# Kernel tuning notes

Hardware: AMD Instinct MI355X
Metric: run time of the kernel (lower is better)

Reference implementation:

```python
import jax, jax.numpy as jnp
import numpy as np


def _l2norm(v, eps=1e-12):
    # torch F.normalize(dim=-1): v / clamp(||v||_2, min=eps)
    n = jnp.linalg.norm(v, axis=-1, keepdims=True)
    return v / jnp.maximum(n, eps)


def setup_inputs() -> dict:
    key = jax.random.key(0)
    ks = jax.random.split(key, 10)
    B, T, N, Ci, E, K, H = 64, 12, 1024, 64, 16, 3, 192
    O = H // 3  # subhidden size
    return {
        "x": jax.random.normal(ks[0], (B, N, Ci), jnp.float32),
        "x_window": jax.random.normal(ks[1], (B, T, N, 1), jnp.float32),
        "node_embeddings": jax.random.normal(ks[2], (N, E), jnp.float32) * 0.1,
        "ZPI": jax.random.normal(ks[3], (B, 3), jnp.float32),
        "supports_adj": jax.random.uniform(ks[4], (K, N, N), jnp.float32),
        "weights_pool": jax.random.normal(ks[5], (E, K, Ci, O), jnp.float32) * 0.1,
        "weights_pool_adj": jax.random.normal(ks[6], (E, K, Ci, O), jnp.float32) * 0.1,
        "weights_window": jax.random.normal(ks[7], (E, 1, O), jnp.float32) * 0.1,
        "bias_pool": jax.random.normal(ks[8], (E, H), jnp.float32) * 0.1,
        "T_param": jax.random.normal(ks[9], (T,), jnp.float32) * 0.1,
    }


def reference(x, x_window, node_embeddings, ZPI, supports_adj,
              weights_pool, weights_pool_adj, weights_window, bias_pool, T_param):
    N = node_embeddings.shape[0]
    K = weights_pool.shape[1]  # link_len

    # adaptive supports: softmax(relu(E E^T)) and its power series
    supports = jax.nn.softmax(jax.nn.relu(node_embeddings @ node_embeddings.T), axis=1)
    support_set = [jnp.eye(N, dtype=x.dtype), supports]
    for k in range(2, K):
        support_set.append(supports @ support_set[k - 1])
    S = jnp.stack(support_set, axis=0)  # (K, N, N)

    # per-node dynamic weights / bias
    weights = jnp.einsum('nd,dkio->nkio', node_embeddings, weights_pool)
    bias = node_embeddings @ bias_pool  # (N, H)

    # adaptive graph conv branch
    x_g = jnp.einsum('knm,bmc->bnkc', S, x)
    x_gconv = _l2norm(jnp.einsum('bnki,nkio->bno', x_g, weights))

    # static adjacency branch ('knn' repeated index = diagonal; sum over m --
    # faithful to the original torch einsum)
    weights_adj = jnp.einsum('nd,dkio->nkio', node_embeddings, weights_pool_adj)
    x_a = jnp.einsum('knn,bmc->bnkc', supports_adj, x)
    x_aconv = _l2norm(jnp.einsum('bnki,nkio->bno', x_a, weights_adj))

    # temporal window branch
    ww = jnp.einsum('nd,dio->nio', node_embeddings, weights_window)  # (N, 1, O)
    x_w = jnp.einsum('btni,nio->btno', x_window, ww)
    x_wconv = _l2norm(jnp.einsum('btno,t->bno', x_w, T_param))

    return jnp.concatenate([x_gconv, x_aconv, x_wconv], axis=-1) + bias
```

## Files before the change

### kernel.cpp

```cpp
#include <hip/hip_runtime.h>


typedef __attribute__((ext_vector_type(4))) float f32x4;
typedef __attribute__((ext_vector_type(8))) short short8;

#define DEVI static __device__ __forceinline__

DEVI float bf2f(short u) {
    unsigned int x = ((unsigned int)(unsigned short)u) << 16;
    return __builtin_bit_cast(float, x);
}
DEVI short f2bf(float f) {
    unsigned int x = __builtin_bit_cast(unsigned int, f);
    x = (x + 0x7FFFu + ((x >> 16) & 1u)) >> 16;
    return (short)(unsigned short)x;
}
DEVI int swz(int row) { return ((row ^ (row >> 3)) & 7) << 3; }

DEVI f32x4 mfma16(short8 a, short8 b, f32x4 c) {
    return __builtin_amdgcn_mfma_f32_16x16x32_bf16(a, b, c, 0, 0, 0);
}

__global__ __launch_bounds__(256) void k_supports(const float* __restrict__ NE,
                                                  short* __restrict__ A_bf) {
    int n = blockIdx.x, t = threadIdx.x;
    __shared__ float En[16];
    __shared__ float wsum[4];
    if (t < 16) En[t] = NE[n * 16 + t];
    __syncthreads();
    float e[4];
    float loc = 0.f;
#pragma unroll
    for (int i = 0; i < 4; ++i) {
        int m = t + 256 * i;
        const float* rp = NE + m * 16;
        float v = 0.f;
#pragma unroll
        for (int d = 0; d < 16; ++d) v += En[d] * rp[d];
        v = fmaxf(v, 0.f);
        e[i] = __expf(v);
        loc += e[i];
    }
#pragma unroll
    for (int off = 32; off; off >>= 1) loc += __shfl_xor(loc, off);
    if ((t & 63) == 0) wsum[t >> 6] = loc;
    __syncthreads();
    float inv = 1.f / (wsum[0] + wsum[1] + wsum[2] + wsum[3]);
#pragma unroll
    for (int i = 0; i < 4; ++i) A_bf[n * 1024 + t + 256 * i] = f2bf(e[i] * inv);
}

__global__ __launch_bounds__(256) void k_small(
        const float* __restrict__ x, const float* __restrict__ xw,
        const float* __restrict__ NE, const float* __restrict__ adj,
        const float* __restrict__ wp, const float* __restrict__ wpa,
        const float* __restrict__ Tp,
        short* __restrict__ B2, short* __restrict__ A2,
        float* __restrict__ xsp, float* __restrict__ s_bn) {
    __shared__ float red[4][64];
    int bid = blockIdx.x, t = threadIdx.x;
    if (bid < 64) {
        int o = bid, j = t;
        short row[64];
        if (j < 192) {
            int kk = j >> 6, i = j & 63;
#pragma unroll
            for (int d = 0; d < 16; ++d)
                row[d] = f2bf(wp[((d * 3 + kk) * 64 + i) * 64 + o]);
#pragma unroll
            for (int k = 16; k < 64; ++k) row[k] = 0;
        } else {
            int i2 = j - 192;
#pragma unroll
            for (int k = 0; k < 16; ++k) row[k] = 0;
#pragma unroll
            for (int d = 0; d < 16; ++d)
#pragma unroll
                for (int kk = 0; kk < 3; ++kk)
                    row[16 + d * 3 + kk] = f2bf(wpa[((d * 3 + kk) * 64 + i2) * 64 + o]);
        }
        short* dst = B2 + (o * 256 + j) * 64;
#pragma unroll
        for (int q = 0; q < 8; ++q) {
            short8 v;
#pragma unroll
            for (int e2 = 0; e2 < 8; ++e2) v[e2] = row[q * 8 + e2];
            *reinterpret_cast<short8*>(dst + q * 8) = v;
        }
    } else if (bid < 320) {
        int idx = bid - 64, b = idx >> 2, mq = idx & 3;
        int c = t & 63, q2 = t >> 6;
        int m0 = mq * 256 + q2 * 64;
        float s = 0.f;
        for (int mm = 0; mm < 64; ++mm) s += x[(b * 1024 + m0 + mm) * 64 + c];
        red[q2][c] = s;
        __syncthreads();
        if (t < 64) xsp[(b * 4 + mq) * 64 + t] = red[0][t] + red[1][t] + red[2][t] + red[3][t];
    } else if (bid < 336) {
        int idx = bid - 320;
        float tp[12];
#pragma unroll
        for (int i = 0; i < 12; ++i) tp[i] = Tp[i];
        for (int bb = 0; bb < 4; ++bb) {
            int b = idx * 4 + bb;
#pragma unroll
            for (int j2 = 0; j2 < 4; ++j2) {
                int nn = t + 256 * j2;
                float s = 0.f;
#pragma unroll
                for (int tt = 0; tt < 12; ++tt) s += xw[(b * 12 + tt) * 1024 + nn] * tp[tt];
                s_bn[b * 1024 + nn] = s;
            }
        }
    } else {
        int n = (bid - 336) * 256 + t;
        float En[16];
#pragma unroll
        for (int d = 0; d < 16; ++d) En[d] = NE[n * 16 + d];
        float dg[3];
#pragma unroll
        for (int k = 0; k < 3; ++k) dg[k] = adj[k * 1024 * 1024 + n * 1024 + n];
        short row[64];
#pragma unroll
        for (int d = 0; d < 16; ++d) row[d] = f2bf(En[d]);
#pragma unroll
        for (int d = 0; d < 16; ++d)
#pragma unroll
            for (int k = 0; k < 3; ++k) row[16 + d * 3 + k] = f2bf(En[d] * dg[k]);
        short* dst = A2 + n * 64;
#pragma unroll
        for (int q = 0; q < 8; ++q) {
            short8 v;
#pragma unroll
            for (int e2 = 0; e2 < 8; ++e2) v[e2] = row[q * 8 + e2];
            *reinterpret_cast<short8*>(dst + q * 8) = v;
        }
    }
}

__global__ __launch_bounds__(256) void k_gemm_w(const short* __restrict__ A2,
                                                const short* __restrict__ B2,
                                                short* __restrict__ Wall) {
    int bx = blockIdx.x, by = blockIdx.y;
    __shared__ __align__(16) short As[128 * 64];
    __shared__ __align__(16) short Bs[128 * 64];
    int t = threadIdx.x;
#pragma unroll
    for (int i = 0; i < 4; ++i) {
        int slot = t + 256 * i;
        int row = slot >> 3, k8 = slot & 7;
        int sw = swz(row);
        short8 va = *reinterpret_cast<const short8*>(A2 + (by * 128 + row) * 64 + k8 * 8);
        *reinterpret_cast<short8*>(&As[row * 64 + ((k8 * 8) ^ sw)]) = va;
        short8 vb = *reinterpret_cast<const short8*>(B2 + (bx * 128 + row) * 64 + k8 * 8);
        *reinterpret_cast<short8*>(&Bs[row * 64 + ((k8 * 8) ^ sw)]) = vb;
    }
    __syncthreads();
    int w = t >> 6, l = t & 63;
    int wm = w & 1, wn = w >> 1;
    int lr = l & 15, lg = l >> 4;
    f32x4 acc[4][4] = {};
#pragma unroll
    for (int ks = 0; ks < 2; ++ks) {
        int kk = ks * 32 + lg * 8;
        short8 af[4], bfr[4];
#pragma unroll
        for (int mf = 0; mf < 4; ++mf) {
            int row = wm * 64 + mf * 16 + lr;
            af[mf] = *reinterpret_cast<const short8*>(&As[row * 64 + (kk ^ swz(row))]);
        }
#pragma unroll
        for (int nf = 0; nf < 4; ++nf) {
            int row = wn * 64 + nf * 16 + lr;
            bfr[nf] = *reinterpret_cast<const short8*>(&Bs[row * 64 + (kk ^ swz(row))]);
        }
#pragma unroll
        for (int mf = 0; mf < 4; ++mf)
#pragma unroll
            for (int nf = 0; nf < 4; ++nf)
                acc[mf][nf] = mfma16(af[mf], bfr[nf], acc[mf][nf]);
    }
#pragma unroll
    for (int mf = 0; mf < 4; ++mf)
#pragma unroll
        for (int nf = 0; nf < 4; ++nf)
#pragma unroll
            for (int r = 0; r < 4; ++r) {
                int row = by * 128 + wm * 64 + mf * 16 + lg * 4 + r;
                int col = bx * 128 + wn * 64 + nf * 16 + lr;
                Wall[row * 16384 + col] = f2bf(acc[mf][nf][r]);
            }
}

template <int BF32>
__global__ __launch_bounds__(256) void k_gemm(const short* __restrict__ A_bf,
                                              const void* __restrict__ Bsrc,
                                              short* __restrict__ Crm) {
    int n0 = blockIdx.x * 128, b = blockIdx.y;
    __shared__ __align__(16) short As[128 * 64];
    __shared__ __align__(16) short Bs[64 * 64];
    int t = threadIdx.x;
    int w = t >> 6, l = t & 63;
    int wm = w & 1, wn = w >> 1;
    int lr = l & 15, lg = l >> 4;
    f32x4 acc[4][2] = {};
    const float* Bf = reinterpret_cast<const float*>(Bsrc) + b * 65536;
    const short* Bh = reinterpret_cast<const short*>(Bsrc) + b * 65536;
    int arow = t >> 3, ak8 = t & 7;
    int bc0 = (t & 7) * 8, bm = t >> 3;
    for (int kt = 0; kt < 16; ++kt) {
#pragma unroll
        for (int i = 0; i < 4; ++i) {
            int row = arow + 32 * i;
            short8 v = *reinterpret_cast<const short8*>(
                A_bf + (n0 + row) * 1024 + kt * 64 + ak8 * 8);
            *reinterpret_cast<short8*>(&As[row * 64 + ((ak8 * 8) ^ swz(row))]) = v;
        }
#pragma unroll
        for (int it = 0; it < 2; ++it) {
            int m = bm + 32 * it;
            if (BF32) {
                const float4* p = reinterpret_cast<const float4*>(Bf + (kt * 64 + m) * 64 + bc0);
                float4 p0 = p[0], p1 = p[1];
                float vv[8] = {p0.x, p0.y, p0.z, p0.w, p1.x, p1.y, p1.z, p1.w};
#pragma unroll
                for (int j = 0; j < 8; ++j) {
                    int c = bc0 + j;
                    Bs[c * 64 + (m ^ swz(c))] = f2bf(vv[j]);
                }
            } else {
                short8 hv = *reinterpret_cast<const short8*>(Bh + (kt * 64 + m) * 64 + bc0);
#pragma unroll
                for (int j = 0; j < 8; ++j) {
                    int c = bc0 + j;
                    Bs[c * 64 + (m ^ swz(c))] = hv[j];
                }
            }
        }
        __syncthreads();
#pragma unroll
        for (int ks = 0; ks < 2; ++ks) {
            int kk = ks * 32 + lg * 8;
            short8 af[4], bfr[2];
#pragma unroll
            for (int mf = 0; mf < 4; ++mf) {
                int row = wm * 64 + mf * 16 + lr;
                af[mf] = *reinterpret_cast<const short8*>(&As[row * 64 + (kk ^ swz(row))]);
            }
#pragma unroll
            for (int nf = 0; nf < 2; ++nf) {
                int c = wn * 32 + nf * 16 + lr;
                bfr[nf] = *reinterpret_cast<const short8*>(&Bs[c * 64 + (kk ^ swz(c))]);
            }
#pragma unroll
            for (int mf = 0; mf < 4; ++mf)
#pragma unroll
                for (int nf = 0; nf < 2; ++nf)
                    acc[mf][nf] = mfma16(af[mf], bfr[nf], acc[mf][nf]);
        }
        __syncthreads();
    }
#pragma unroll
    for (int mf = 0; mf < 4; ++mf)
#pragma unroll
        for (int nf = 0; nf < 2; ++nf)
#pragma unroll
            for (int r = 0; r < 4; ++r) {
                int nrow = n0 + wm * 64 + mf * 16 + lg * 4 + r;
                int c = wn * 32 + nf * 16 + lr;
                Crm[(b * 1024 + nrow) * 64 + c] = f2bf(acc[mf][nf][r]);
            }
}

__global__ __launch_bounds__(256) void k_epi(
        const float* __restrict__ x, const short* __restrict__ y1,
        const short* __restrict__ y2, const float* __restrict__ xsp,
        const float* __restrict__ s_bn, const short* __restrict__ Wall,
        const float* __restrict__ NE, const float* __restrict__ bp,
        const float* __restrict__ wwin, float* __restrict__ out) {
    int n = blockIdx.x, t = threadIdx.x;
    __shared__ __align__(16) short Ylds[64 * 256];
    __shared__ float E_l[16];
    __shared__ float bias_l[192];
    __shared__ float ww_l[64];
    __shared__ float sq_l[2][2][64];
    __shared__ float wwn_l;
    if (t < 16) E_l[t] = NE[n * 16 + t];
    __syncthreads();
    if (t < 192) {
        float s = 0.f;
#pragma unroll
        for (int d = 0; d < 16; ++d) s += E_l[d] * bp[d * 192 + t];
        bias_l[t] = s;
    } else {
        int o = t - 192;
        float s = 0.f;
#pragma unroll
        for (int d = 0; d < 16; ++d) s += E_l[d] * wwin[d * 64 + o];
        ww_l[o] = s;
    }
    int w = t >> 6, l = t & 63;
    int wm = w & 1, wn = w >> 1;
    int lr = l & 15, lg = l >> 4;
    short8 wf[8][2];
#pragma unroll
    for (int ks = 0; ks < 8; ++ks)
#pragma unroll
        for (int nf = 0; nf < 2; ++nf) {
            int o = wn * 32 + nf * 16 + lr;
            int k = ks * 32 + lg * 8;
            wf[ks][nf] = *reinterpret_cast<const short8*>(Wall + (n * 64 + o) * 256 + k);
        }
    for (int it = 0; it < 16; ++it) {
        int b = it * 4 + (t >> 6);
        int c = t & 63;
        int sw = swz(b);
        int base = b * 256;
        float xv = x[(b * 1024 + n) * 64 + c];
        short y1v = y1[(b * 1024 + n) * 64 + c];
        short y2v = y2[(b * 1024 + n) * 64 + c];
        float xs = xsp[(b * 4 + 0) * 64 + c] + xsp[(b * 4 + 1) * 64 + c] +
                   xsp[(b * 4 + 2) * 64 + c] + xsp[(b * 4 + 3) * 64 + c];
        Ylds[base + ((0 * 64 + c) ^ sw)] = f2bf(xv);
        Ylds[base + ((1 * 64 + c) ^ sw)] = y1v;
        Ylds[base + ((2 * 64 + c) ^ sw)] = y2v;
        Ylds[base + ((3 * 64 + c) ^ sw)] = f2bf(xs);
    }
    __syncthreads();
    if (t < 64) {
        float v = ww_l[t];
        float s2 = v * v;
#pragma unroll
        for (int off = 32; off; off >>= 1) s2 += __shfl_xor(s2, off);
        if (t == 0) wwn_l = sqrtf(s2);
    }
    f32x4 accg[2][2] = {};
    f32x4 acca[2][2] = {};
#pragma unroll
    for (int ks = 0; ks < 8; ++ks) {
        short8 af[2];
#pragma unroll
        for (int mf = 0; mf < 2; ++mf) {
            int b = wm * 32 + mf * 16 + lr;
            int k = ks * 32 + lg * 8;
            af[mf] = *reinterpret_cast<const short8*>(&Ylds[b * 256 + (k ^ swz(b))]);
        }
#pragma unroll
        for (int mf = 0; mf < 2; ++mf)
#pragma unroll
            for (int nf = 0; nf < 2; ++nf) {
                if (ks < 6) accg[mf][nf] = mfma16(af[mf], wf[ks][nf], accg[mf][nf]);
                else        acca[mf][nf] = mfma16(af[mf], wf[ks][nf], acca[mf][nf]);
            }
    }
#pragma unroll
    for (int mf = 0; mf < 2; ++mf)
#pragma unroll
        for (int r = 0; r < 4; ++r) {
            float sg = accg[mf][0][r] * accg[mf][0][r] + accg[mf][1][r] * accg[mf][1][r];
            float sa = acca[mf][0][r] * acca[mf][0][r] + acca[mf][1][r] * acca[mf][1][r];
#pragma unroll
            for (int off = 1; off < 16; off <<= 1) {
                sg += __shfl_xor(sg, off);
                sa += __shfl_xor(sa, off);
            }
            if (lr == 0) {
                int b = wm * 32 + mf * 16 + lg * 4 + r;
                sq_l[0][wn][b] = sg;
                sq_l[1][wn][b] = sa;
            }
        }
    __syncthreads();
#pragma unroll
    for (int mf = 0; mf < 2; ++mf)
#pragma unroll
        for (int r = 0; r < 4; ++r) {
            int b = wm * 32 + mf * 16 + lg * 4 + r;
            float ig = 1.f / fmaxf(sqrtf(sq_l[0][0][b] + sq_l[0][1][b]), 1e-12f);
            float ia = 1.f / fmaxf(sqrtf(sq_l[1][0][b] + sq_l[1][1][b]), 1e-12f);
            float* po = out + (b * 1024 + n) * 192;
#pragma unroll
            for (int nf = 0; nf < 2; ++nf) {
                int o = wn * 32 + nf * 16 + lr;
                po[o]      = accg[mf][nf][r] * ig + bias_l[o];
                po[64 + o] = acca[mf][nf][r] * ia + bias_l[64 + o];
            }
        }
    float wwn = wwn_l;
    for (int it = 0; it < 16; ++it) {
        int b = it * 4 + (t >> 6);
        int o = t & 63;
        float s = s_bn[b * 1024 + n];
        float pre = s * ww_l[o];
        float nrm = fabsf(s) * wwn;
        out[(b * 1024 + n) * 192 + 128 + o] = pre / fmaxf(nrm, 1e-12f) + bias_l[128 + o];
    }
}

extern "C" void kernel_launch(void* const* d_in, const int* in_sizes, int n_in,
                              void* d_out, int out_size, void* d_ws, size_t ws_size,
                              hipStream_t stream) {
    const float* x    = (const float*)d_in[0];
    const float* xw   = (const float*)d_in[1];
    const float* NE   = (const float*)d_in[2];
    const float* adj  = (const float*)d_in[4];
    const float* wp   = (const float*)d_in[5];
    const float* wpa  = (const float*)d_in[6];
    const float* wwin = (const float*)d_in[7];
    const float* bp   = (const float*)d_in[8];
    const float* Tp   = (const float*)d_in[9];
    float* out = (float*)d_out;

    char* ws = (char*)d_ws;
    const size_t OFF_ABF  = 0;
    const size_t OFF_Y1   = 2097152;
    const size_t OFF_Y2   = 10485760;
    const size_t OFF_WALL = 18874368;
    const size_t OFF_A2   = 52428800;
    const size_t OFF_B2   = 52559872;
    const size_t OFF_XSP  = 54657024;
    const size_t OFF_SBN  = 54722560;
    const size_t NEED     = 54984704;
    if (ws_size < NEED) return;

    short* A_bf = (short*)(ws + OFF_ABF);
    short* y1   = (short*)(ws + OFF_Y1);
    short* y2   = (short*)(ws + OFF_Y2);
    short* Wall = (short*)(ws + OFF_WALL);
    short* A2   = (short*)(ws + OFF_A2);
    short* B2   = (short*)(ws + OFF_B2);
    float* xsp  = (float*)(ws + OFF_XSP);
    float* s_bn = (float*)(ws + OFF_SBN);

    k_supports<<<1024, 256, 0, stream>>>(NE, A_bf);
    k_small<<<340, 256, 0, stream>>>(x, xw, NE, adj, wp, wpa, Tp, B2, A2, xsp, s_bn);
    k_gemm_w<<<dim3(128, 8), 256, 0, stream>>>(A2, B2, Wall);
    k_gemm<1><<<dim3(8, 64), 256, 0, stream>>>(A_bf, (const void*)x, y1);
    k_gemm<0><<<dim3(8, 64), 256, 0, stream>>>(A_bf, (const void*)y1, y2);
    k_epi<<<1024, 256, 0, stream>>>(x, y1, y2, xsp, s_bn, Wall, NE, bp, wwin, out);
}
```

Baseline: 107.3 us.

## Precompute S squared and batch both graph-conv GEMMs into one wide GEMM

Replaces the two dependent per-batch GEMMs (S·x, then S·y1) with an explicit S·S GEMM followed by a single large GEMM [S; S²]·Xᵀ, where batch and channel are folded into one 4096-wide N dimension. A new prep kernel transposes S and x to bf16 and pre-reduces the xs term. The GEMMs load tiles straight into LDS with global_load_lds, and the epilogue now uses vectorized short8 loads. This removes the serial dependency between the two GEMMs and gives larger, better-shaped tiles. In exchange it does more total FLOPs, adds transpose traffic, and the unswizzled LDS layout may cause bank conflicts.

```diff
diff --git a/kernel.cpp b/kernel.cpp
--- a/kernel.cpp
+++ b/kernel.cpp
@@ -6,10 +6,6 @@
 
 #define DEVI static __device__ __forceinline__
 
-DEVI float bf2f(short u) {
-    unsigned int x = ((unsigned int)(unsigned short)u) << 16;
-    return __builtin_bit_cast(float, x);
-}
 DEVI short f2bf(float f) {
     unsigned int x = __builtin_bit_cast(unsigned int, f);
     x = (x + 0x7FFFu + ((x >> 16) & 1u)) >> 16;
@@ -21,8 +17,14 @@
     return __builtin_amdgcn_mfma_f32_16x16x32_bf16(a, b, c, 0, 0, 0);
 }
 
+DEVI void gload16(const void* g, void* l) {
+    __builtin_amdgcn_global_load_lds(
+        (const __attribute__((address_space(1))) unsigned int*)g,
+        (__attribute__((address_space(3))) unsigned int*)l, 16, 0, 0);
+}
+
 __global__ __launch_bounds__(256) void k_supports(const float* __restrict__ NE,
-                                                  short* __restrict__ A_bf) {
+                                                  short* __restrict__ S) {
     int n = blockIdx.x, t = threadIdx.x;
     __shared__ float En[16];
     __shared__ float wsum[4];
@@ -47,7 +49,7 @@
     __syncthreads();
     float inv = 1.f / (wsum[0] + wsum[1] + wsum[2] + wsum[3]);
 #pragma unroll
-    for (int i = 0; i < 4; ++i) A_bf[n * 1024 + t + 256 * i] = f2bf(e[i] * inv);
+    for (int i = 0; i < 4; ++i) S[n * 1024 + t + 256 * i] = f2bf(e[i] * inv);
 }
 
 __global__ __launch_bounds__(256) void k_small(
@@ -138,6 +140,128 @@
     }
 }
 
+__global__ __launch_bounds__(256) void k_prep(const float* __restrict__ x,
+                                              const short* __restrict__ S,
+                                              const float* __restrict__ xsp,
+                                              short* __restrict__ ST,
+                                              short* __restrict__ XT,
+                                              short* __restrict__ xs_bf) {
+    __shared__ __align__(16) short Tbuf[64 * 128];
+    int bid = blockIdx.x, t = threadIdx.x;
+    if (bid < 512) {
+        int b = bid >> 3, m0 = (bid & 7) * 128;
+        const float* xp = x + ((size_t)b * 1024 + m0) * 64;
+#pragma unroll
+        for (int p = 0; p < 8; ++p) {
+            int idx = t + 256 * p;
+            int r = idx >> 4, c4 = (idx & 15) * 4;
+            float4 v = *reinterpret_cast<const float4*>(&xp[r * 64 + c4]);
+            Tbuf[(c4 + 0) * 128 + r] = f2bf(v.x);
+            Tbuf[(c4 + 1) * 128 + r] = f2bf(v.y);
+            Tbuf[(c4 + 2) * 128 + r] = f2bf(v.z);
+            Tbuf[(c4 + 3) * 128 + r] = f2bf(v.w);
+        }
+        __syncthreads();
+#pragma unroll
+        for (int p = 0; p < 4; ++p) {
+            int idx = t + 256 * p;
+            int c = idx >> 4, q = idx & 15;
+            *reinterpret_cast<short8*>(&XT[((size_t)b * 64 + c) * 1024 + m0 + q * 8]) =
+                *reinterpret_cast<const short8*>(&Tbuf[c * 128 + q * 8]);
+        }
+    } else if (bid < 768) {
+        int idx = bid - 512, bi = idx >> 4, bj = idx & 15;
+        int c8 = (t & 7) * 8;
+#pragma unroll
+        for (int p = 0; p < 2; ++p) {
+            int r = (t >> 3) + 32 * p;
+            short8 v = *reinterpret_cast<const short8*>(
+                &S[(size_t)(bi * 64 + r) * 1024 + bj * 64 + c8]);
+#pragma unroll
+            for (int e = 0; e < 8; ++e) Tbuf[(c8 + e) * 64 + r] = v[e];
+        }
+        __syncthreads();
+#pragma unroll
+        for (int p = 0; p < 2; ++p) {
+            int r = (t >> 3) + 32 * p;
+            *reinterpret_cast<short8*>(&ST[(size_t)(bj * 64 + r) * 1024 + bi * 64 + c8]) =
+                *reinterpret_cast<const short8*>(&Tbuf[r * 64 + c8]);
+        }
+    } else {
+        int j = (bid - 768) * 256 + t;
+        int b = j >> 6, c = j & 63;
+        float s = xsp[(b * 4 + 0) * 64 + c] + xsp[(b * 4 + 1) * 64 + c] +
+                  xsp[(b * 4 + 2) * 64 + c] + xsp[(b * 4 + 3) * 64 + c];
+        xs_bf[j] = f2bf(s);
+    }
+}
+
+DEVI void mm_tile(const short* __restrict__ A, const short* __restrict__ Bt,
+                  short* __restrict__ C, int ldC) {
+    __shared__ __align__(16) short As[128 * 64];
+    __shared__ __align__(16) short Bs[128 * 64];
+    int t = threadIdx.x, wid = t >> 6, lane = t & 63;
+    int rsub = lane >> 3, csub = (lane & 7) * 8;
+    int wm = wid & 1, wn = wid >> 1;
+    int lr = lane & 15, lg = lane >> 4;
+    f32x4 acc[4][4] = {};
+    for (int kt = 0; kt < 16; ++kt) {
+#pragma unroll
+        for (int q = 0; q < 4; ++q) {
+            int row = q * 32 + wid * 8;
+            gload16(A + (size_t)(row + rsub) * 1024 + kt * 64 + csub, As + row * 64);
+            gload16(Bt + (size_t)(row + rsub) * 1024 + kt * 64 + csub, Bs + row * 64);
+        }
+        __syncthreads();
+#pragma unroll
+        for (int ks = 0; ks < 2; ++ks) {
+            int kk = ks * 32 + lg * 8;
+            short8 af[4], bfv[4];
+#pragma unroll
+            for (int i = 0; i < 4; ++i)
+                af[i] = *reinterpret_cast<const short8*>(&As[(wm * 64 + i * 16 + lr) * 64 + kk]);
+#pragma unroll
+            for (int i = 0; i < 4; ++i)
+                bfv[i] = *reinterpret_cast<const short8*>(&Bs[(wn * 64 + i * 16 + lr) * 64 + kk]);
+#pragma unroll
+            for (int mf = 0; mf < 4; ++mf)
+#pragma unroll
+                for (int nf = 0; nf < 4; ++nf)
+                    acc[mf][nf] = mfma16(af[mf], bfv[nf], acc[mf][nf]);
+        }
+        __syncthreads();
+    }
+#pragma unroll
+    for (int mf = 0; mf < 4; ++mf)
+#pragma unroll
+        for (int nf = 0; nf < 4; ++nf)
+#pragma unroll
+            for (int r = 0; r < 4; ++r) {
+                int g = wm * 64 + mf * 16 + lg * 4 + r;
+                int j = wn * 64 + nf * 16 + lr;
+                C[(size_t)g * ldC + j] = f2bf(acc[mf][nf][r]);
+            }
+}
+
+__global__ __launch_bounds__(256) void k_gemmS2(const short* __restrict__ S,
+                                                const short* __restrict__ ST,
+                                                short* __restrict__ S2) {
+    int bx = blockIdx.x, by = blockIdx.y;
+    mm_tile(S + (size_t)by * 128 * 1024, ST + (size_t)bx * 128 * 1024,
+            S2 + (size_t)by * 128 * 1024 + bx * 128, 1024);
+}
+
+__global__ __launch_bounds__(256) void k_gemmY(const short* __restrict__ S,
+                                               const short* __restrict__ S2,
+                                               const short* __restrict__ XT,
+                                               short* __restrict__ Y) {
+    int bx = blockIdx.x, by = blockIdx.y;
+    const short* A = (by < 8) ? (S + (size_t)by * 128 * 1024)
+                              : (S2 + (size_t)(by - 8) * 128 * 1024);
+    mm_tile(A, XT + (size_t)bx * 128 * 1024,
+            Y + (size_t)by * 128 * 4096 + bx * 128, 4096);
+}
+
 __global__ __launch_bounds__(256) void k_gemm_w(const short* __restrict__ A2,
                                                 const short* __restrict__ B2,
                                                 short* __restrict__ Wall) {
@@ -188,96 +312,16 @@
             for (int r = 0; r < 4; ++r) {
                 int row = by * 128 + wm * 64 + mf * 16 + lg * 4 + r;
                 int col = bx * 128 + wn * 64 + nf * 16 + lr;
-                Wall[row * 16384 + col] = f2bf(acc[mf][nf][r]);
-            }
-}
-
-template <int BF32>
-__global__ __launch_bounds__(256) void k_gemm(const short* __restrict__ A_bf,
-                                              const void* __restrict__ Bsrc,
-                                              short* __restrict__ Crm) {
-    int n0 = blockIdx.x * 128, b = blockIdx.y;
-    __shared__ __align__(16) short As[128 * 64];
-    __shared__ __align__(16) short Bs[64 * 64];
-    int t = threadIdx.x;
-    int w = t >> 6, l = t & 63;
-    int wm = w & 1, wn = w >> 1;
-    int lr = l & 15, lg = l >> 4;
-    f32x4 acc[4][2] = {};
-    const float* Bf = reinterpret_cast<const float*>(Bsrc) + b * 65536;
-    const short* Bh = reinterpret_cast<const short*>(Bsrc) + b * 65536;
-    int arow = t >> 3, ak8 = t & 7;
-    int bc0 = (t & 7) * 8, bm = t >> 3;
-    for (int kt = 0; kt < 16; ++kt) {
-#pragma unroll
-        for (int i = 0; i < 4; ++i) {
-            int row = arow + 32 * i;
-            short8 v = *reinterpret_cast<const short8*>(
-                A_bf + (n0 + row) * 1024 + kt * 64 + ak8 * 8);
-            *reinterpret_cast<short8*>(&As[row * 64 + ((ak8 * 8) ^ swz(row))]) = v;
-        }
-#pragma unroll
-        for (int it = 0; it < 2; ++it) {
-            int m = bm + 32 * it;
-            if (BF32) {
-                const float4* p = reinterpret_cast<const float4*>(Bf + (kt * 64 + m) * 64 + bc0);
-                float4 p0 = p[0], p1 = p[1];
-                float vv[8] = {p0.x, p0.y, p0.z, p0.w, p1.x, p1.y, p1.z, p1.w};
-#pragma unroll
-                for (int j = 0; j < 8; ++j) {
-                    int c = bc0 + j;
-                    Bs[c * 64 + (m ^ swz(c))] = f2bf(vv[j]);
-                }
-            } else {
-                short8 hv = *reinterpret_cast<const short8*>(Bh + (kt * 64 + m) * 64 + bc0);
-#pragma unroll
-                for (int j = 0; j < 8; ++j) {
-                    int c = bc0 + j;
-                    Bs[c * 64 + (m ^ swz(c))] = hv[j];
-                }
-            }
-        }
-        __syncthreads();
-#pragma unroll
-        for (int ks = 0; ks < 2; ++ks) {
-            int kk = ks * 32 + lg * 8;
-            short8 af[4], bfr[2];
-#pragma unroll
-            for (int mf = 0; mf < 4; ++mf) {
-                int row = wm * 64 + mf * 16 + lr;
-                af[mf] = *reinterpret_cast<const short8*>(&As[row * 64 + (kk ^ swz(row))]);
-            }
-#pragma unroll
-            for (int nf = 0; nf < 2; ++nf) {
-                int c = wn * 32 + nf * 16 + lr;
-                bfr[nf] = *reinterpret_cast<const short8*>(&Bs[c * 64 + (kk ^ swz(c))]);
-            }
-#pragma unroll
-            for (int mf = 0; mf < 4; ++mf)
-#pragma unroll
-                for (int nf = 0; nf < 2; ++nf)
-                    acc[mf][nf] = mfma16(af[mf], bfr[nf], acc[mf][nf]);
-        }
-        __syncthreads();
-    }
-#pragma unroll
-    for (int mf = 0; mf < 4; ++mf)
-#pragma unroll
-        for (int nf = 0; nf < 2; ++nf)
-#pragma unroll
-            for (int r = 0; r < 4; ++r) {
-                int nrow = n0 + wm * 64 + mf * 16 + lg * 4 + r;
-                int c = wn * 32 + nf * 16 + lr;
-                Crm[(b * 1024 + nrow) * 64 + c] = f2bf(acc[mf][nf][r]);
+                Wall[(size_t)row * 16384 + col] = f2bf(acc[mf][nf][r]);
             }
 }
 
 __global__ __launch_bounds__(256) void k_epi(
-        const float* __restrict__ x, const short* __restrict__ y1,
-        const short* __restrict__ y2, const float* __restrict__ xsp,
-        const float* __restrict__ s_bn, const short* __restrict__ Wall,
-        const float* __restrict__ NE, const float* __restrict__ bp,
-        const float* __restrict__ wwin, float* __restrict__ out) {
+        const float* __restrict__ x, const short* __restrict__ Y,
+        const short* __restrict__ xs_bf, const float* __restrict__ s_bn,
+        const short* __restrict__ Wall, const float* __restrict__ NE,
+        const float* __restrict__ bp, const float* __restrict__ wwin,
+        float* __restrict__ out) {
     int n = blockIdx.x, t = threadIdx.x;
     __shared__ __align__(16) short Ylds[64 * 256];
     __shared__ float E_l[16];
@@ -309,22 +353,29 @@
         for (int nf = 0; nf < 2; ++nf) {
             int o = wn * 32 + nf * 16 + lr;
             int k = ks * 32 + lg * 8;
-            wf[ks][nf] = *reinterpret_cast<const short8*>(Wall + (n * 64 + o) * 256 + k);
-        }
-    for (int it = 0; it < 16; ++it) {
-        int b = it * 4 + (t >> 6);
-        int c = t & 63;
-        int sw = swz(b);
-        int base = b * 256;
-        float xv = x[(b * 1024 + n) * 64 + c];
-        short y1v = y1[(b * 1024 + n) * 64 + c];
-        short y2v = y2[(b * 1024 + n) * 64 + c];
-        float xs = xsp[(b * 4 + 0) * 64 + c] + xsp[(b * 4 + 1) * 64 + c] +
-                   xsp[(b * 4 + 2) * 64 + c] + xsp[(b * 4 + 3) * 64 + c];
-        Ylds[base + ((0 * 64 + c) ^ sw)] = f2bf(xv);
-        Ylds[base + ((1 * 64 + c) ^ sw)] = y1v;
-        Ylds[base + ((2 * 64 + c) ^ sw)] = y2v;
-        Ylds[base + ((3 * 64 + c) ^ sw)] = f2bf(xs);
+            wf[ks][nf] = *reinterpret_cast<const short8*>(Wall + ((size_t)n * 64 + o) * 256 + k);
+        }
+    const short* y1r = Y + (size_t)n * 4096;
+    const short* y2r = Y + (size_t)(1024 + n) * 4096;
+#pragma unroll
+    for (int it = 0; it < 8; ++it) {
+        int part = it >> 1;
+        int b = (it & 1) * 32 + (t >> 3);
+        int q = t & 7;
+        short8 v;
+        if (part == 0) {
+            const float4* p = reinterpret_cast<const float4*>(&x[((size_t)b * 1024 + n) * 64 + q * 8]);
+            float4 p0 = p[0], p1 = p[1];
+            v[0] = f2bf(p0.x); v[1] = f2bf(p0.y); v[2] = f2bf(p0.z); v[3] = f2bf(p0.w);
+            v[4] = f2bf(p1.x); v[5] = f2bf(p1.y); v[6] = f2bf(p1.z); v[7] = f2bf(p1.w);
+        } else if (part == 1) {
+            v = *reinterpret_cast<const short8*>(&y1r[b * 64 + q * 8]);
+        } else if (part == 2) {
+            v = *reinterpret_cast<const short8*>(&y2r[b * 64 + q * 8]);
+        } else {
+            v = *reinterpret_cast<const short8*>(&xs_bf[b * 64 + q * 8]);
+        }
+        *reinterpret_cast<short8*>(&Ylds[b * 256 + ((part * 64 + q * 8) ^ swz(b))]) = v;
     }
     __syncthreads();
     if (t < 64) {
@@ -378,7 +429,7 @@
             int b = wm * 32 + mf * 16 + lg * 4 + r;
             float ig = 1.f / fmaxf(sqrtf(sq_l[0][0][b] + sq_l[0][1][b]), 1e-12f);
             float ia = 1.f / fmaxf(sqrtf(sq_l[1][0][b] + sq_l[1][1][b]), 1e-12f);
-            float* po = out + (b * 1024 + n) * 192;
+            float* po = out + ((size_t)b * 1024 + n) * 192;
 #pragma unroll
             for (int nf = 0; nf < 2; ++nf) {
                 int o = wn * 32 + nf * 16 + lr;
@@ -387,13 +438,14 @@
             }
         }
     float wwn = wwn_l;
+#pragma unroll
     for (int it = 0; it < 16; ++it) {
         int b = it * 4 + (t >> 6);
         int o = t & 63;
         float s = s_bn[b * 1024 + n];
         float pre = s * ww_l[o];
         float nrm = fabsf(s) * wwn;
-        out[(b * 1024 + n) * 192 + 128 + o] = pre / fmaxf(nrm, 1e-12f) + bias_l[128 + o];
+        out[((size_t)b * 1024 + n) * 192 + 128 + o] = pre / fmaxf(nrm, 1e-12f) + bias_l[128 + o];
     }
 }
 
@@ -412,30 +464,37 @@
     float* out = (float*)d_out;
 
     char* ws = (char*)d_ws;
-    const size_t OFF_ABF  = 0;
-    const size_t OFF_Y1   = 2097152;
-    const size_t OFF_Y2   = 10485760;
-    const size_t OFF_WALL = 18874368;
-    const size_t OFF_A2   = 52428800;
-    const size_t OFF_B2   = 52559872;
-    const size_t OFF_XSP  = 54657024;
-    const size_t OFF_SBN  = 54722560;
-    const size_t NEED     = 54984704;
+    const size_t OFF_S    = 0;
+    const size_t OFF_ST   = 2097152;
+    const size_t OFF_S2   = 4194304;
+    const size_t OFF_XT   = 6291456;
+    const size_t OFF_WALL = 0;
+    const size_t OFF_Y    = 33554432;
+    const size_t OFF_A2   = 50331648;
+    const size_t OFF_B2   = 50462720;
+    const size_t OFF_XSP  = 52559872;
+    const size_t OFF_XSBF = 52625408;
+    const size_t OFF_SBN  = 52633600;
+    const size_t NEED     = 52895744;
     if (ws_size < NEED) return;
 
-    short* A_bf = (short*)(ws + OFF_ABF);
-    short* y1   = (short*)(ws + OFF_Y1);
-    short* y2   = (short*)(ws + OFF_Y2);
-    short* Wall = (short*)(ws + OFF_WALL);
-    short* A2   = (short*)(ws + OFF_A2);
-    short* B2   = (short*)(ws + OFF_B2);
-    float* xsp  = (float*)(ws + OFF_XSP);
-    float* s_bn = (float*)(ws + OFF_SBN);
-
-    k_supports<<<1024, 256, 0, stream>>>(NE, A_bf);
+    short* S     = (short*)(ws + OFF_S);
+    short* ST    = (short*)(ws + OFF_ST);
+    short* S2    = (short*)(ws + OFF_S2);
+    short* XT    = (short*)(ws + OFF_XT);
+    short* Wall  = (short*)(ws + OFF_WALL);
+    short* Y     = (short*)(ws + OFF_Y);
+    short* A2    = (short*)(ws + OFF_A2);
+    short* B2    = (short*)(ws + OFF_B2);
+    float* xsp   = (float*)(ws + OFF_XSP);
+    short* xs_bf = (short*)(ws + OFF_XSBF);
+    float* s_bn  = (float*)(ws + OFF_SBN);
+
+    k_supports<<<1024, 256, 0, stream>>>(NE, S);
     k_small<<<340, 256, 0, stream>>>(x, xw, NE, adj, wp, wpa, Tp, B2, A2, xsp, s_bn);
+    k_prep<<<784, 256, 0, stream>>>(x, S, xsp, ST, XT, xs_bf);
+    k_gemmS2<<<dim3(8, 8), 256, 0, stream>>>(S, ST, S2);
+    k_gemmY<<<dim3(32, 16), 256, 0, stream>>>(S, S2, XT, Y);
     k_gemm_w<<<dim3(128, 8), 256, 0, stream>>>(A2, B2, Wall);
-    k_gemm<1><<<dim3(8, 64), 256, 0, stream>>>(A_bf, (const void*)x, y1);
-    k_gemm<0><<<dim3(8, 64), 256, 0, stream>>>(A_bf, (const void*)y1, y2);
-    k_epi<<<1024, 256, 0, stream>>>(x, y1, y2, xsp, s_bn, Wall, NE, bp, wwin, out);
-}
+    k_epi<<<1024, 256, 0, stream>>>(x, Y, xs_bf, s_bn, Wall, NE, bp, wwin, out);
+}
```

Result: slower. 118.7 us (+10.5%).
